# Kernel optimization log

Measured on AMD Instinct MI355X. Metric: run time of the kernel, lower is better.

Reference implementation:

```python
import jax, jax.numpy as jnp
import numpy as np

B, T = 16, 32768
N_FILTERS, FILTER_LEN = 30, 7


def _stable_coeffs(rng, n_filters, k):
    """Stable IIR denominators (a[0]=1, poles inside unit circle) + random numerators."""
    order = k - 1
    as_list = []
    for _ in range(n_filters):
        radii = rng.uniform(0.5, 0.95, order // 2)
        angles = rng.uniform(0.05, np.pi - 0.05, order // 2)
        poles = radii * np.exp(1j * angles)
        poles = np.concatenate([poles, poles.conj()])
        as_list.append(np.poly(poles).real)  # length k, a[0]=1
    as_ = np.stack(as_list).astype(np.float32)
    bs = (rng.normal(size=(n_filters, k)) * 0.1).astype(np.float32)
    return bs, as_


def setup_inputs() -> dict:
    key = jax.random.key(0)
    x = jax.random.normal(key, (B, T), dtype=jnp.float32)
    rng = np.random.default_rng(0)
    bs, as_ = _stable_coeffs(rng, N_FILTERS, FILTER_LEN)
    return {"x": x, "bs": jnp.asarray(bs), "as_": jnp.asarray(as_)}


def reference(x, bs, as_):
    # x: [B, T]; bs, as_: [F, K]. Output: [B, F, T]
    F, K = bs.shape
    Bb, Tt = x.shape
    a0 = as_[:, :1]
    b = bs / a0
    a_rest = (as_ / a0)[:, 1:]  # [F, K-1]

    # FIR part: fir[b,f,t] = sum_k b[f,k] * x[b, t-k]  (causal convolution)
    lhs = x[:, None, :]                      # [B, 1, T]
    kern = jnp.flip(b, axis=1)[:, None, :]   # [F, 1, K] (flip: conv, not corr)
    fir = jax.lax.conv_general_dilated(
        lhs, kern, window_strides=(1,), padding=[(K - 1, 0)],
        dimension_numbers=("NCH", "OIH", "NCH"))  # [B, F, T]

    # Recursive part: y[t] = fir[t] - sum_{k=1..K-1} a[k] * y[t-k]
    def step(ybuf, fir_t):
        # ybuf: [B, F, K-1] holds y[t-1], ..., y[t-(K-1)]
        y_t = fir_t - jnp.einsum("bfk,fk->bf", ybuf, a_rest)
        ybuf = jnp.concatenate([y_t[:, :, None], ybuf[:, :, :-1]], axis=2)
        return ybuf, y_t

    init = jnp.zeros((Bb, F, K - 1), dtype=x.dtype)
    _, ys = jax.lax.scan(step, init, jnp.moveaxis(fir, 2, 0))  # ys: [T, B, F]
    return jnp.transpose(ys, (1, 2, 0))  # [B, F, T]
```

## Files before the change

### kernel.cpp

```cpp
#include <hip/hip_runtime.h>


#define BB 16
#define TT 32768
#define FF 30
#define KK 7
#define ORD 6
#define CHUNK 64
#define CPB 2
#define TSPAN (CPB * CHUNK)
#define NBC (TT / TSPAN)
#define WARM 128
#define XTILE (WARM + TSPAN)
#define YSTR 68
#define BLK 64

__device__ __forceinline__ float iir_step(float xv, float st[ORD],
                                          const float bcf[KK],
                                          const float acf[ORD]) {
    float y = fmaf(bcf[0], xv, st[0]);
#pragma unroll
    for (int j = 0; j < ORD - 1; ++j)
        st[j] = fmaf(-acf[j], y, fmaf(bcf[j + 1], xv, st[j + 1]));
    st[ORD - 1] = fmaf(-acf[ORD - 1], y, bcf[KK - 1] * xv);
    return y;
}

__global__ __launch_bounds__(BLK, 4) void iir_occ_kernel(
    const float* __restrict__ x,
    const float* __restrict__ bs,
    const float* __restrict__ as_,
    float* __restrict__ out)
{
    __shared__ __align__(16) float ly[FF * YSTR];
    __shared__ __align__(16) float lx[XTILE];

    const int tid = threadIdx.x;
    const int b   = blockIdx.x / NBC;
    const int bc  = blockIdx.x % NBC;
    const int bt0 = bc * TSPAN;

    const int f  = tid % FF;
    const int cl = tid / FF;
    const bool active = tid < FF * CPB;

    float bcf[KK], acf[ORD];
    {
        const int fc = active ? f : 0;
        const float inv_a0 = 1.0f / as_[fc * KK];
#pragma unroll
        for (int j = 0; j < KK; ++j) bcf[j] = bs[fc * KK + j] * inv_a0;
#pragma unroll
        for (int j = 0; j < ORD; ++j) acf[j] = as_[fc * KK + 1 + j] * inv_a0;
    }

    {
        const float* __restrict__ xrow = x + b * TT;
        const int t = bt0 - WARM + 4 * tid;
        float4 v = make_float4(0.f, 0.f, 0.f, 0.f);
        if (t >= 0) v = *reinterpret_cast<const float4*>(xrow + t);
        *reinterpret_cast<float4*>(lx + 4 * tid) = v;
    }
    __syncthreads();

    float4 yreg[16];
    if (active) {
        const float4* lx4 = reinterpret_cast<const float4*>(lx);
        const int g0 = 16 * cl;
        float st[ORD];
#pragma unroll
        for (int j = 0; j < ORD; ++j) st[j] = 0.0f;

#pragma unroll
        for (int k = 0; k < 48; ++k) {
            const float4 v = lx4[g0 + k];
            float4 y;
            y.x = iir_step(v.x, st, bcf, acf);
            y.y = iir_step(v.y, st, bcf, acf);
            y.z = iir_step(v.z, st, bcf, acf);
            y.w = iir_step(v.w, st, bcf, acf);
            if (k >= 32) yreg[k - 32] = y;
        }
    }

    float* __restrict__ obase0 = out + b * FF * TT + bt0;
#pragma unroll
    for (int p = 0; p < CPB; ++p) {
        if (active && cl == p) {
            float* lyc = ly + f * YSTR;
#pragma unroll
            for (int k = 0; k < 16; ++k)
                *reinterpret_cast<float4*>(lyc + 4 * k) = yreg[k];
        }
        __syncthreads();

        float* __restrict__ obase = obase0 + p * CHUNK;
#pragma unroll
        for (int i = 0; i < 8; ++i) {
            const int j = i * BLK + tid;
            if (j < FF * (CHUNK / 4)) {
                const int fr = j >> 4;
                const int tl = (j & 15) << 2;
                const float4 v =
                    *reinterpret_cast<const float4*>(ly + fr * YSTR + tl);
                *reinterpret_cast<float4*>(obase + fr * TT + tl) = v;
            }
        }
        __syncthreads();
    }
}

extern "C" void kernel_launch(void* const* d_in, const int* in_sizes, int n_in,
                              void* d_out, int out_size, void* d_ws,
                              size_t ws_size, hipStream_t stream) {
    const float* x   = (const float*)d_in[0];
    const float* bs  = (const float*)d_in[1];
    const float* as_ = (const float*)d_in[2];
    float* out = (float*)d_out;

    const int grid = BB * NBC;
    hipLaunchKernelGGL(iir_occ_kernel, dim3(grid), dim3(BLK), 0, stream,
                       x, bs, as_, out);
}
```

Baseline: 25.69 us.

## Double per-thread chunk length to halve warm-up overhead, stream output in two phases

Each thread now filters a 128-sample chunk after the same 128-sample warm-up instead of a 64-sample chunk, so the redundant warm-up recursion is amortised over twice as many outputs. The block count halves. Outputs are produced in two 64-sample phases, each staged through shared memory and written out with coalesced stores, so register usage stays bounded. In exchange the per-thread serial chain is longer, there are fewer blocks to hide latency, launch bounds drop to 2 waves, and shared memory grows.

```diff
diff --git a/kernel.cpp b/kernel.cpp
--- a/kernel.cpp
+++ b/kernel.cpp
@@ -6,13 +6,13 @@
 #define FF 30
 #define KK 7
 #define ORD 6
-#define CHUNK 64
+#define LCH 128
+#define WARM 128
 #define CPB 2
-#define TSPAN (CPB * CHUNK)
+#define TSPAN (CPB * LCH)
 #define NBC (TT / TSPAN)
-#define WARM 128
+#define YSTR 68
 #define XTILE (WARM + TSPAN)
-#define YSTR 68
 #define BLK 64
 
 __device__ __forceinline__ float iir_step(float xv, float st[ORD],
@@ -26,13 +26,13 @@
     return y;
 }
 
-__global__ __launch_bounds__(BLK, 4) void iir_occ_kernel(
+__global__ __launch_bounds__(BLK, 2) void iir_r18_kernel(
     const float* __restrict__ x,
     const float* __restrict__ bs,
     const float* __restrict__ as_,
     float* __restrict__ out)
 {
-    __shared__ __align__(16) float ly[FF * YSTR];
+    __shared__ __align__(16) float ly[CPB * FF * YSTR];
     __shared__ __align__(16) float lx[XTILE];
 
     const int tid = threadIdx.x;
@@ -56,55 +56,66 @@
 
     {
         const float* __restrict__ xrow = x + b * TT;
-        const int t = bt0 - WARM + 4 * tid;
-        float4 v = make_float4(0.f, 0.f, 0.f, 0.f);
-        if (t >= 0) v = *reinterpret_cast<const float4*>(xrow + t);
-        *reinterpret_cast<float4*>(lx + 4 * tid) = v;
+#pragma unroll
+        for (int i = 0; i < 2; ++i) {
+            const int p = i * BLK + tid;
+            if (p < XTILE / 4) {
+                const int t = bt0 - WARM + 4 * p;
+                float4 v = make_float4(0.f, 0.f, 0.f, 0.f);
+                if (t >= 0) v = *reinterpret_cast<const float4*>(xrow + t);
+                *reinterpret_cast<float4*>(lx + 4 * p) = v;
+            }
+        }
     }
     __syncthreads();
 
-    float4 yreg[16];
+    const float4* lx4 = reinterpret_cast<const float4*>(lx);
+    const int g0 = 32 * cl;
+    float st[ORD];
+#pragma unroll
+    for (int j = 0; j < ORD; ++j) st[j] = 0.0f;
+    float* lyc = ly + (cl * FF + f) * YSTR;
+
     if (active) {
-        const float4* lx4 = reinterpret_cast<const float4*>(lx);
-        const int g0 = 16 * cl;
-        float st[ORD];
 #pragma unroll
-        for (int j = 0; j < ORD; ++j) st[j] = 0.0f;
-
-#pragma unroll
-        for (int k = 0; k < 48; ++k) {
+        for (int k = 0; k < 32; ++k) {
             const float4 v = lx4[g0 + k];
-            float4 y;
-            y.x = iir_step(v.x, st, bcf, acf);
-            y.y = iir_step(v.y, st, bcf, acf);
-            y.z = iir_step(v.z, st, bcf, acf);
-            y.w = iir_step(v.w, st, bcf, acf);
-            if (k >= 32) yreg[k - 32] = y;
+            iir_step(v.x, st, bcf, acf);
+            iir_step(v.y, st, bcf, acf);
+            iir_step(v.z, st, bcf, acf);
+            iir_step(v.w, st, bcf, acf);
         }
     }
 
-    float* __restrict__ obase0 = out + b * FF * TT + bt0;
+    float* __restrict__ obase = out + b * FF * TT + bt0;
+
 #pragma unroll
-    for (int p = 0; p < CPB; ++p) {
-        if (active && cl == p) {
-            float* lyc = ly + f * YSTR;
+    for (int ph = 0; ph < 2; ++ph) {
+        if (active) {
 #pragma unroll
-            for (int k = 0; k < 16; ++k)
-                *reinterpret_cast<float4*>(lyc + 4 * k) = yreg[k];
+            for (int k = 0; k < 16; ++k) {
+                const float4 v = lx4[g0 + 32 + 16 * ph + k];
+                float4 y;
+                y.x = iir_step(v.x, st, bcf, acf);
+                y.y = iir_step(v.y, st, bcf, acf);
+                y.z = iir_step(v.z, st, bcf, acf);
+                y.w = iir_step(v.w, st, bcf, acf);
+                *reinterpret_cast<float4*>(lyc + 4 * k) = y;
+            }
         }
         __syncthreads();
 
-        float* __restrict__ obase = obase0 + p * CHUNK;
 #pragma unroll
-        for (int i = 0; i < 8; ++i) {
-            const int j = i * BLK + tid;
-            if (j < FF * (CHUNK / 4)) {
-                const int fr = j >> 4;
-                const int tl = (j & 15) << 2;
-                const float4 v =
-                    *reinterpret_cast<const float4*>(ly + fr * YSTR + tl);
-                *reinterpret_cast<float4*>(obase + fr * TT + tl) = v;
-            }
+        for (int i = 0; i < 15; ++i) {
+            const int j  = i * BLK + tid;
+            const int c  = j / (FF * 16);
+            const int r  = j % (FF * 16);
+            const int fr = r >> 4;
+            const int k  = r & 15;
+            const float4 v = *reinterpret_cast<const float4*>(
+                ly + (c * FF + fr) * YSTR + 4 * k);
+            *reinterpret_cast<float4*>(
+                obase + fr * TT + c * LCH + ph * 64 + 4 * k) = v;
         }
         __syncthreads();
     }
@@ -119,6 +130,6 @@
     float* out = (float*)d_out;
 
     const int grid = BB * NBC;
-    hipLaunchKernelGGL(iir_occ_kernel, dim3(grid), dim3(BLK), 0, stream,
+    hipLaunchKernelGGL(iir_r18_kernel, dim3(grid), dim3(BLK), 0, stream,
                        x, bs, as_, out);
 }
```

New measurement: 24.00 us, median of 2. -6.6%, faster.
